# Optimization experiments

Hardware: AMD Instinct MI355X
Metric: run time of the kernel (lower is better)

Reference implementation:

```python
import jax, jax.numpy as jnp
import numpy as np

LN_EPS = 1e-5

def _layer_norm(x, g, b):
    m = jnp.mean(x, axis=-1, keepdims=True)
    v = jnp.mean((x - m) ** 2, axis=-1, keepdims=True)
    return (x - m) / jnp.sqrt(v + LN_EPS) * g + b

def setup_inputs() -> dict:
    key = jax.random.key(0)
    ks = jax.random.split(key, 16)
    B, L, D = 4, 2048, 1024
    DF = 4 * D
    s_in = 1.0 / np.sqrt(D)
    s_ff = 1.0 / np.sqrt(DF)
    # torch init of phazor: exp(2j*pi*arange(D)/D) * |randn|
    ang = 2.0 * np.pi * jnp.arange(D, dtype=jnp.float32) / D
    mag = jnp.abs(jax.random.normal(ks[0], (D,), jnp.float32))
    return {
        "x": jax.random.normal(ks[1], (B, L, D), jnp.float32),
        "hidden_real": jax.random.normal(ks[2], (B, D), jnp.float32),
        "hidden_imag": jax.random.normal(ks[3], (B, D), jnp.float32),
        "phazor_real": mag * jnp.cos(ang),
        "phazor_imag": mag * jnp.sin(ang),
        "phazor_init_real": jax.random.normal(ks[4], (D,), jnp.float32),
        "phazor_init_imag": jax.random.normal(ks[5], (D,), jnp.float32),
        "ln_gamma": jnp.ones((D,), jnp.float32),
        "ln_beta": jnp.zeros((D,), jnp.float32),
        "fc_w": jax.random.uniform(ks[6], (D, D), jnp.float32, -s_in, s_in),
        "fc_b": jax.random.uniform(ks[7], (D,), jnp.float32, -s_in, s_in),
        "w1": jax.random.uniform(ks[8], (DF, D), jnp.float32, -s_in, s_in),
        "b1": jax.random.uniform(ks[9], (DF,), jnp.float32, -s_in, s_in),
        "w2": jax.random.uniform(ks[10], (D, DF), jnp.float32, -s_ff, s_ff),
        "b2": jax.random.uniform(ks[11], (D,), jnp.float32, -s_ff, s_ff),
    }

def _spiral_conv(x, hidden, phazor_p, phazor_init):
    # x: [B,L,D] real, hidden: [B,D] complex
    B, L, D = x.shape
    amag = jnp.abs(phazor_p)
    phazor = phazor_p / amag * jnp.exp(-amag)                      # [D]
    prog = jnp.power(phazor[None, :], jnp.arange(L)[:, None])      # [L,D]
    filt = prog * phazor_init[None, :]                             # [L,D]
    filt_fft = jnp.fft.fft(filt, n=2 * L, axis=0)                  # [2L,D]
    x_fft = jnp.fft.fft(x.astype(jnp.complex64), n=2 * L, axis=1)  # [B,2L,D]
    conv = jnp.fft.ifft(filt_fft[None] * x_fft, axis=1)[:, :L]     # [B,L,D]
    conv_with_past = conv + jax.lax.stop_gradient(hidden)[:, None, :] * prog[None] * phazor[None, None]
    return conv_with_past.real, conv_with_past

def reference(x, hidden_real, hidden_imag, phazor_real, phazor_imag,
              phazor_init_real, phazor_init_imag, ln_gamma, ln_beta,
              fc_w, fc_b, w1, b1, w2, b2):
    hidden = hidden_real + 1j * hidden_imag
    phazor_p = phazor_real + 1j * phazor_imag
    phazor_init = phazor_init_real + 1j * phazor_init_imag

    x_res = x
    xn = _layer_norm(x, ln_gamma, ln_beta)
    s, new_hidden = _spiral_conv(xn, hidden, phazor_p, phazor_init)
    y = jax.nn.silu(jnp.einsum('bld,ed->ble', x, fc_w) + fc_b)
    h = s * y + x_res                      # dropout is identity (p=0 / eval)
    hn = _layer_norm(h, ln_gamma, ln_beta) # same LayerNorm instance reused
    ffn = jnp.einsum('blf,df->bld', jax.nn.silu(jnp.einsum('bld,fd->blf', hn, w1) + b1), w2) + b2
    out = ffn + h
    return out, new_hidden
```

## Files before the change

### kernel.cpp

```cpp
#include <hip/hip_runtime.h>

typedef unsigned short u16;
typedef unsigned int u32;
typedef float f32x4 __attribute__((ext_vector_type(4)));
typedef __bf16 bf16x8 __attribute__((ext_vector_type(8)));

__device__ __forceinline__ float b2f(u16 u) {
    return __uint_as_float(((u32)u) << 16);
}
__device__ __forceinline__ u16 f2b(float f) {
    u32 u = __float_as_uint(f);
    return (u16)((u + 0x7FFFu + ((u >> 16) & 1u)) >> 16);
}
__device__ __forceinline__ bool is_f32(const u32* flag) {
    return flag[0] == 0x3F800000u;
}
__device__ __forceinline__ float lda(const void* p, size_t i, bool f) {
    return f ? ((const float*)p)[i] : b2f(((const u16*)p)[i]);
}
__device__ __forceinline__ void cmul(float& xr, float& xi, float yr, float yi) {
    float tr = xr * yr - xi * yi;
    xi = xr * yi + xi * yr;
    xr = tr;
}
__device__ __forceinline__ void gl2lds16(const void* g, void* l) {
    __builtin_amdgcn_global_load_lds(
        (const __attribute__((address_space(1))) void*)g,
        (__attribute__((address_space(3))) void*)l, 16, 0, 0);
}
__device__ __forceinline__ void wg_barrier() {
    asm volatile("" ::: "memory");
    __builtin_amdgcn_sched_barrier(0);
    __builtin_amdgcn_s_barrier();
    __builtin_amdgcn_sched_barrier(0);
    asm volatile("" ::: "memory");
}
#define VWAIT0 { asm volatile("s_waitcnt vmcnt(0)" ::: "memory"); __builtin_amdgcn_sched_barrier(0); }
#define VWAIT6 { asm volatile("s_waitcnt vmcnt(6)" ::: "memory"); __builtin_amdgcn_sched_barrier(0); }

__global__ __launch_bounds__(256) void cvt_k(const void* __restrict__ src,
                                             u32* __restrict__ dst, int n2,
                                             const u32* __restrict__ flag) {
    bool f = is_f32(flag);
    int i = blockIdx.x * 256 + threadIdx.x;
    if (i >= n2) return;
    if (f) {
        float2 v = ((const float2*)src)[i];
        dst[i] = (u32)f2b(v.x) | ((u32)f2b(v.y) << 16);
    } else {
        dst[i] = ((const u32*)src)[i];
    }
}

__global__ __launch_bounds__(256) void ln_k(const u16* __restrict__ x,
                                            const u16* __restrict__ g,
                                            const u16* __restrict__ be,
                                            u16* __restrict__ o, int D) {
    int row = blockIdx.x;
    const u16* xr = x + (size_t)row * D;
    int tid = threadIdx.x;
    float s = 0.f, s2 = 0.f;
    for (int i = tid; i < D; i += 256) {
        float v = b2f(xr[i]);
        s += v; s2 += v * v;
    }
    for (int off = 32; off > 0; off >>= 1) {
        s  += __shfl_down(s,  off, 64);
        s2 += __shfl_down(s2, off, 64);
    }
    __shared__ float red[8];
    int wave = tid >> 6;
    if ((tid & 63) == 0) { red[wave * 2] = s; red[wave * 2 + 1] = s2; }
    __syncthreads();
    if (tid == 0) {
        float ts = 0.f, ts2 = 0.f;
        for (int w = 0; w < 4; w++) { ts += red[w * 2]; ts2 += red[w * 2 + 1]; }
        float m = ts / D;
        float v = ts2 / D - m * m;
        red[0] = m;
        red[1] = rsqrtf(v + 1e-5f);
    }
    __syncthreads();
    float m = red[0], inv = red[1];
    u16* orow = o + (size_t)row * D;
    for (int i = tid; i < D; i += 256) {
        float v = (b2f(xr[i]) - m) * inv * b2f(g[i]) + b2f(be[i]);
        orow[i] = f2b(v);
    }
}

__global__ __launch_bounds__(256) void scan_partial_k(const u16* __restrict__ xn,
                                                      const void* __restrict__ phr_,
                                                      const void* __restrict__ phi_,
                                                      float2* __restrict__ T,
                                                      int L, int D, int C, int Kc,
                                                      const u32* __restrict__ flag) {
    bool f = is_f32(flag);
    int tid = blockIdx.x * 256 + threadIdx.x;
    int d = tid % D;
    int c = (tid / D) % C;
    int b = tid / (D * C);
    float pr = lda(phr_, d, f), pi = lda(phi_, d, f);
    float amag = fmaxf(sqrtf(pr * pr + pi * pi), 1e-12f);
    float sc = __expf(-amag) / amag;
    float phr = pr * sc, phi = pi * sc;
    float Tr = 0.f, Ti = 0.f;
    const u16* xp = xn + ((size_t)b * L + (size_t)c * Kc) * D + d;
    for (int t = 0; t < Kc; t++) {
        float x = b2f(xp[(size_t)t * D]);
        float nr = phr * Tr - phi * Ti + x;
        Ti = phr * Ti + phi * Tr;
        Tr = nr;
    }
    T[tid] = make_float2(Tr, Ti);
}

__global__ __launch_bounds__(256) void scan_prefix_k(const void* __restrict__ phr_,
                                                     const void* __restrict__ phi_,
                                                     const float2* __restrict__ T,
                                                     float2* __restrict__ E,
                                                     int D, int C,
                                                     const u32* __restrict__ flag) {
    bool f = is_f32(flag);
    int tid = blockIdx.x * 256 + threadIdx.x;
    int d = tid % D;
    int b = tid / D;
    float pr = lda(phr_, d, f), pi = lda(phi_, d, f);
    float amag = fmaxf(sqrtf(pr * pr + pi * pi), 1e-12f);
    float sc = __expf(-amag) / amag;
    float phr = pr * sc, phi = pi * sc;
    float kr = phr, ki = phi;
    for (int s = 0; s < 7; s++) cmul(kr, ki, kr, ki);
    float cr = 0.f, ci = 0.f;
    for (int c = 0; c < C; c++) {
        size_t i = ((size_t)b * C + c) * D + d;
        E[i] = make_float2(cr, ci);
        float2 t = T[i];
        cmul(cr, ci, kr, ki);
        cr += t.x; ci += t.y;
    }
}

__global__ __launch_bounds__(256) void scan_final_k(const u16* __restrict__ xn,
                                                    const void* __restrict__ phr_,
                                                    const void* __restrict__ phi_,
                                                    const void* __restrict__ pir_,
                                                    const void* __restrict__ pii_,
                                                    const void* __restrict__ hr_,
                                                    const void* __restrict__ hi_,
                                                    const float2* __restrict__ E,
                                                    u16* __restrict__ sws,
                                                    void* __restrict__ dout,
                                                    int MD, int out_elems,
                                                    int L, int D, int C, int Kc,
                                                    const u32* __restrict__ flag) {
    bool f = is_f32(flag);
    int tid = blockIdx.x * 256 + threadIdx.x;
    int d = tid % D;
    int c = (tid / D) % C;
    int b = tid / (D * C);
    float pr = lda(phr_, d, f), pi = lda(phi_, d, f);
    float amag = fmaxf(sqrtf(pr * pr + pi * pi), 1e-12f);
    float sc = __expf(-amag) / amag;
    float phr = pr * sc, phi = pi * sc;
    float kr = phr, ki = phi;
    for (int s = 0; s < 7; s++) cmul(kr, ki, kr, ki);
    float Pr = phr, Pi = phi;
    for (int j = 0; j < c; j++) cmul(Pr, Pi, kr, ki);
    float ir = lda(pir_, d, f), ii = lda(pii_, d, f);
    float hr = lda(hr_, (size_t)b * D + d, f), hi = lda(hi_, (size_t)b * D + d, f);
    float2 e = E[tid];
    float Sr = e.x, Si = e.y;
    const bool full = (out_elems >= 3 * MD);
    size_t mbase = (size_t)b * L + (size_t)c * Kc;
    for (int t = 0; t < Kc; t++) {
        size_t off = (mbase + t) * D + d;
        float x = b2f(xn[off]);
        float nr = phr * Sr - phi * Si + x;
        Si = phr * Si + phi * Sr;
        Sr = nr;
        float cr = ir * Sr - ii * Si + hr * Pr - hi * Pi;
        float ci = ir * Si + ii * Sr + hr * Pi + hi * Pr;
        sws[off] = f2b(cr);
        if (f) {
            float* fo = (float*)dout;
            if (full) {
                fo[(size_t)MD + 2 * off]     = cr;
                fo[(size_t)MD + 2 * off + 1] = ci;
            } else {
                fo[(size_t)MD + off] = cr;
            }
        } else {
            u16* uo = (u16*)dout;
            if (full) {
                uo[(size_t)MD + 2 * off]     = f2b(cr);
                uo[(size_t)MD + 2 * off + 1] = f2b(ci);
            } else {
                uo[(size_t)MD + off] = f2b(cr);
            }
        }
        cmul(Pr, Pi, phr, phi);
    }
}

template <int MODE>
__global__ __launch_bounds__(512) void gemm_nt(const u16* __restrict__ A,
                                               const u16* __restrict__ Bm,
                                               int M, int N, int K,
                                               const u16* __restrict__ bias,
                                               const u16* __restrict__ sbuf,
                                               const u16* __restrict__ xbuf,
                                               u16* __restrict__ out,
                                               void* __restrict__ outv,
                                               const u32* __restrict__ flag) {
    __shared__ u16 As[3][128 * 64];
    __shared__ u16 Bs[3][256 * 64];
    const int tid = threadIdx.x;
    const int wave = tid >> 6, lane = tid & 63;
    const int quad = lane >> 4, l16 = lane & 15;

    const int NT = N >> 8;
    const int j = blockIdx.x;
    const int gsize = 8 * NT;
    const int mg  = j / gsize;
    const int rem = j - mg * gsize;
    const int nt  = rem >> 3;
    const int mi  = rem & 7;
    const int bm = (mg * 8 + mi) * 128, bn = nt * 256;

    const int wrow = (wave >> 2) * 64, wcol = (wave & 3) * 64;

    f32x4 acc[4][4] = {};

    const int lr = lane >> 3;
    const int sl = (lane & 7) ^ lr;
    const size_t goff = (size_t)lr * K + sl * 8;
    const u16* aG = A  + (size_t)(bm + wave * 16) * K + goff;
    const u16* bG = Bm + (size_t)(bn + wave * 32) * K + goff;
    const size_t K8 = (size_t)K * 8;

    u16* aB0 = &As[0][0]; u16* aB1 = &As[1][0]; u16* aB2 = &As[2][0];
    u16* bB0 = &Bs[0][0]; u16* bB1 = &Bs[1][0]; u16* bB2 = &Bs[2][0];

#define STG_P1(aB, bB, t) { \
        const u16* ga = aG + (size_t)(t) * 64; \
        gl2lds16(ga,      (aB) + wave * (16 * 64)); \
        gl2lds16(ga + K8, (aB) + wave * (16 * 64) + 8 * 64); \
        gl2lds16(bG + (size_t)(t) * 64, (bB) + wave * (32 * 64)); }
#define STG_P2(bB, t) { \
        const u16* gb = bG + (size_t)(t) * 64; \
        gl2lds16(gb + K8,     (bB) + wave * (32 * 64) + 8 * 64); \
        gl2lds16(gb + 2 * K8, (bB) + wave * (32 * 64) + 16 * 64); \
        gl2lds16(gb + 3 * K8, (bB) + wave * (32 * 64) + 24 * 64); }

#define RDA(aB, m, ks) (*(const bf16x8*)&(aB)[(wrow + (m) * 16 + l16) * 64 + \
        ((((ks) * 4 + quad) ^ (l16 & 7)) << 3)])
#define RDB(bB, n, ks) (*(const bf16x8*)&(bB)[(wcol + (n) * 16 + l16) * 64 + \
        ((((ks) * 4 + quad) ^ (l16 & 7)) << 3)])

#define FM(mm, nn, ks) acc[mm][nn] = __builtin_amdgcn_mfma_f32_16x16x32_bf16( \
        av[mm][ks], bv[nn][ks], acc[mm][nn], 0, 0, 0)
#define MFMA16(ks) { \
        __builtin_amdgcn_s_setprio(1); \
        FM(0, 0, ks); FM(0, 1, ks); FM(1, 0, ks); FM(1, 1, ks); \
        FM(0, 2, ks); FM(0, 3, ks); FM(1, 2, ks); FM(1, 3, ks); \
        FM(2, 0, ks); FM(2, 1, ks); FM(3, 0, ks); FM(3, 1, ks); \
        FM(2, 2, ks); FM(2, 3, ks); FM(3, 2, ks); FM(3, 3, ks); \
        __builtin_amdgcn_s_setprio(0); }

    bf16x8 av[4][2], bv[4][2];
    const int KT = K >> 6;

    STG_P1(aB0, bB0, 0); STG_P2(bB0, 0);
    STG_P1(aB1, bB1, 1); STG_P2(bB1, 1);
    VWAIT6;
    wg_barrier();

    for (int t = 0; t < KT; ++t) {
        const bool stg = (t + 2 < KT);
        av[0][0] = RDA(aB0, 0, 0); av[1][0] = RDA(aB0, 1, 0);
        av[2][0] = RDA(aB0, 2, 0); av[3][0] = RDA(aB0, 3, 0);
        bv[0][0] = RDB(bB0, 0, 0); bv[1][0] = RDB(bB0, 1, 0);
        bv[2][0] = RDB(bB0, 2, 0); bv[3][0] = RDB(bB0, 3, 0);
        if (stg) STG_P1(aB2, bB2, t + 2);
        wg_barrier();
        MFMA16(0);
        wg_barrier();
        av[0][1] = RDA(aB0, 0, 1); av[1][1] = RDA(aB0, 1, 1);
        av[2][1] = RDA(aB0, 2, 1); av[3][1] = RDA(aB0, 3, 1);
        bv[0][1] = RDB(bB0, 0, 1); bv[1][1] = RDB(bB0, 1, 1);
        bv[2][1] = RDB(bB0, 2, 1); bv[3][1] = RDB(bB0, 3, 1);
        if (stg) STG_P2(bB2, t + 2);
        wg_barrier();
        MFMA16(1);
        if (stg) { VWAIT6 }
        else if (t + 1 < KT) { VWAIT0 }
        wg_barrier();
        u16* ta = aB0; aB0 = aB1; aB1 = aB2; aB2 = ta;
        u16* tb = bB0; bB0 = bB1; bB1 = bB2; bB2 = tb;
    }

    bool f = (MODE == 2) ? is_f32(flag) : false;
#pragma unroll
    for (int mi2 = 0; mi2 < 4; mi2++) {
#pragma unroll
        for (int ni = 0; ni < 4; ni++) {
            int colg = bn + wcol + ni * 16 + l16;
            float bsv = b2f(bias[colg]);
#pragma unroll
            for (int r = 0; r < 4; r++) {
                int rowg = bm + wrow + mi2 * 16 + quad * 4 + r;
                size_t idx = (size_t)rowg * N + colg;
                float v = acc[mi2][ni][r] + bsv;
                if (MODE == 0) {
                    float y = v / (1.f + __expf(-v));
                    float hv = b2f(sbuf[idx]) * y + b2f(xbuf[idx]);
                    out[idx] = f2b(hv);
                } else if (MODE == 1) {
                    float y = v / (1.f + __expf(-v));
                    out[idx] = f2b(y);
                } else {
                    float o = v + b2f(xbuf[idx]);
                    if (f) ((float*)outv)[idx] = o;
                    else   ((u16*)outv)[idx] = f2b(o);
                }
            }
        }
    }
#undef STG_P1
#undef STG_P2
#undef RDA
#undef RDB
#undef FM
#undef MFMA16
}

extern "C" void kernel_launch(void* const* d_in, const int* in_sizes, int n_in,
                              void* d_out, int out_size, void* d_ws, size_t ws_size,
                              hipStream_t stream) {
    const void* x   = d_in[0];
    const void* hr  = d_in[1];
    const void* hi  = d_in[2];
    const void* phr = d_in[3];
    const void* phi = d_in[4];
    const void* pir = d_in[5];
    const void* pii = d_in[6];
    const void* g   = d_in[7];
    const void* be  = d_in[8];
    const void* fcw = d_in[9];
    const void* fcb = d_in[10];
    const void* w1  = d_in[11];
    const void* b1  = d_in[12];
    const void* w2  = d_in[13];
    const void* b2  = d_in[14];
    const u32* flag = (const u32*)g;

    const int D  = in_sizes[3];
    const int Bb = in_sizes[1] / D;
    const int L  = in_sizes[0] / (Bb * D);
    const int DF = in_sizes[12];
    const int M  = Bb * L;
    const int Kc = 128, C = L / Kc;
    const int MD = M * D;

    char* ws = (char*)d_ws;
    size_t MD2 = (size_t)MD * 2;
    u16*    xb  = (u16*)(ws);
    u16*    xn  = (u16*)(ws + MD2);
    u16*    sws = (u16*)(ws + 2 * MD2);
    float2* T   = (float2*)(ws + 3 * MD2);
    float2* E   = (float2*)(ws + 3 * MD2 + (size_t)Bb * C * D * 8);
    u16*    a1  = (u16*)(ws);
    u16*    h   = (u16*)(ws + 4 * MD2);
    u16*    hn  = (u16*)(ws + 5 * MD2);
    char*   wp  = ws + 6 * MD2;
    u16* fcwb = (u16*)wp; wp += (size_t)D * D * 2;
    u16* w1b  = (u16*)wp; wp += (size_t)DF * D * 2;
    u16* w2b  = (u16*)wp; wp += (size_t)D * DF * 2;
    u16* fcbb = (u16*)wp; wp += (size_t)D * 2;
    u16* b1b  = (u16*)wp; wp += (size_t)DF * 2;
    u16* b2b  = (u16*)wp; wp += (size_t)D * 2;
    u16* gb   = (u16*)wp; wp += (size_t)D * 2;
    u16* bb   = (u16*)wp; wp += (size_t)D * 2;

    auto cvt = [&](const void* src, u16* dst, size_t n) {
        int n2 = (int)(n / 2);
        cvt_k<<<(n2 + 255) / 256, 256, 0, stream>>>(src, (u32*)dst, n2, flag);
    };
    cvt(x,   xb,   (size_t)MD);
    cvt(fcw, fcwb, (size_t)D * D);
    cvt(w1,  w1b,  (size_t)DF * D);
    cvt(w2,  w2b,  (size_t)D * DF);
    cvt(fcb, fcbb, (size_t)D);
    cvt(b1,  b1b,  (size_t)DF);
    cvt(b2,  b2b,  (size_t)D);
    cvt(g,   gb,   (size_t)D);
    cvt(be,  bb,   (size_t)D);

    ln_k<<<M, 256, 0, stream>>>(xb, gb, bb, xn, D);
    scan_partial_k<<<(Bb * C * D) / 256, 256, 0, stream>>>(xn, phr, phi, T, L, D, C, Kc, flag);
    scan_prefix_k<<<(Bb * D) / 256, 256, 0, stream>>>(phr, phi, T, E, D, C, flag);
    scan_final_k<<<(Bb * C * D) / 256, 256, 0, stream>>>(xn, phr, phi, pir, pii, hr, hi,
                                                         E, sws, d_out, MD, out_size,
                                                         L, D, C, Kc, flag);
    gemm_nt<0><<<(M / 128) * (D / 256), 512, 0, stream>>>(xb, fcwb, M, D, D, fcbb, sws, xb, h, nullptr, flag);
    ln_k<<<M, 256, 0, stream>>>(h, gb, bb, hn, D);
    gemm_nt<1><<<(M / 128) * (DF / 256), 512, 0, stream>>>(hn, w1b, M, DF, D, b1b, nullptr, nullptr, a1, nullptr, flag);
    gemm_nt<2><<<(M / 128) * (D / 256), 512, 0, stream>>>(a1, w2b, M, D, DF, b2b, nullptr, h, nullptr, d_out, flag);
}
```

Before: 472.8 us.

## Unroll GEMM K-loop by three with static LDS buffers and one barrier per step

Replaces the rotating LDS buffer pointers with compile-time buffer indices by unrolling the K loop three ways. Each K step now issues the whole next-stage global-to-LDS copy at once, reads both k-slices of fragments up front, then runs 32 MFMAs behind a single barrier instead of three. This cuts barrier count and pointer arithmetic and may let the compiler schedule LDS reads better. In exchange it uses more registers and code size and waits longer before the first MFMA of each step.

```diff
diff --git a/kernel.cpp b/kernel.cpp
--- a/kernel.cpp
+++ b/kernel.cpp
@@ -239,23 +239,19 @@
     const u16* bG = Bm + (size_t)(bn + wave * 32) * K + goff;
     const size_t K8 = (size_t)K * 8;
 
-    u16* aB0 = &As[0][0]; u16* aB1 = &As[1][0]; u16* aB2 = &As[2][0];
-    u16* bB0 = &Bs[0][0]; u16* bB1 = &Bs[1][0]; u16* bB2 = &Bs[2][0];
-
-#define STG_P1(aB, bB, t) { \
+#define STG(B, t) { \
         const u16* ga = aG + (size_t)(t) * 64; \
-        gl2lds16(ga,      (aB) + wave * (16 * 64)); \
-        gl2lds16(ga + K8, (aB) + wave * (16 * 64) + 8 * 64); \
-        gl2lds16(bG + (size_t)(t) * 64, (bB) + wave * (32 * 64)); }
-#define STG_P2(bB, t) { \
         const u16* gb = bG + (size_t)(t) * 64; \
-        gl2lds16(gb + K8,     (bB) + wave * (32 * 64) + 8 * 64); \
-        gl2lds16(gb + 2 * K8, (bB) + wave * (32 * 64) + 16 * 64); \
-        gl2lds16(gb + 3 * K8, (bB) + wave * (32 * 64) + 24 * 64); }
-
-#define RDA(aB, m, ks) (*(const bf16x8*)&(aB)[(wrow + (m) * 16 + l16) * 64 + \
+        gl2lds16(ga,          &As[B][wave * (16 * 64)]); \
+        gl2lds16(ga + K8,     &As[B][wave * (16 * 64) + 8 * 64]); \
+        gl2lds16(gb,          &Bs[B][wave * (32 * 64)]); \
+        gl2lds16(gb + K8,     &Bs[B][wave * (32 * 64) + 8 * 64]); \
+        gl2lds16(gb + 2 * K8, &Bs[B][wave * (32 * 64) + 16 * 64]); \
+        gl2lds16(gb + 3 * K8, &Bs[B][wave * (32 * 64) + 24 * 64]); }
+
+#define RDA(B, m, ks) (*(const bf16x8*)&As[B][(wrow + (m) * 16 + l16) * 64 + \
         ((((ks) * 4 + quad) ^ (l16 & 7)) << 3)])
-#define RDB(bB, n, ks) (*(const bf16x8*)&(bB)[(wcol + (n) * 16 + l16) * 64 + \
+#define RDB(B, n, ks) (*(const bf16x8*)&Bs[B][(wcol + (n) * 16 + l16) * 64 + \
         ((((ks) * 4 + quad) ^ (l16 & 7)) << 3)])
 
 #define FM(mm, nn, ks) acc[mm][nn] = __builtin_amdgcn_mfma_f32_16x16x32_bf16( \
@@ -268,36 +264,34 @@
         FM(2, 2, ks); FM(2, 3, ks); FM(3, 2, ks); FM(3, 3, ks); \
         __builtin_amdgcn_s_setprio(0); }
 
+#define ITER(RB, SB, t) { \
+        if ((t) + 2 < KT) STG(SB, (t) + 2); \
+        av[0][0] = RDA(RB, 0, 0); av[1][0] = RDA(RB, 1, 0); \
+        av[2][0] = RDA(RB, 2, 0); av[3][0] = RDA(RB, 3, 0); \
+        bv[0][0] = RDB(RB, 0, 0); bv[1][0] = RDB(RB, 1, 0); \
+        bv[2][0] = RDB(RB, 2, 0); bv[3][0] = RDB(RB, 3, 0); \
+        av[0][1] = RDA(RB, 0, 1); av[1][1] = RDA(RB, 1, 1); \
+        av[2][1] = RDA(RB, 2, 1); av[3][1] = RDA(RB, 3, 1); \
+        bv[0][1] = RDB(RB, 0, 1); bv[1][1] = RDB(RB, 1, 1); \
+        bv[2][1] = RDB(RB, 2, 1); bv[3][1] = RDB(RB, 3, 1); \
+        MFMA16(0); \
+        MFMA16(1); \
+        if ((t) + 2 < KT) { VWAIT6 } \
+        else if ((t) + 1 < KT) { VWAIT0 } \
+        wg_barrier(); }
+
     bf16x8 av[4][2], bv[4][2];
     const int KT = K >> 6;
 
-    STG_P1(aB0, bB0, 0); STG_P2(bB0, 0);
-    STG_P1(aB1, bB1, 1); STG_P2(bB1, 1);
+    STG(0, 0);
+    STG(1, 1);
     VWAIT6;
     wg_barrier();
 
-    for (int t = 0; t < KT; ++t) {
-        const bool stg = (t + 2 < KT);
-        av[0][0] = RDA(aB0, 0, 0); av[1][0] = RDA(aB0, 1, 0);
-        av[2][0] = RDA(aB0, 2, 0); av[3][0] = RDA(aB0, 3, 0);
-        bv[0][0] = RDB(bB0, 0, 0); bv[1][0] = RDB(bB0, 1, 0);
-        bv[2][0] = RDB(bB0, 2, 0); bv[3][0] = RDB(bB0, 3, 0);
-        if (stg) STG_P1(aB2, bB2, t + 2);
-        wg_barrier();
-        MFMA16(0);
-        wg_barrier();
-        av[0][1] = RDA(aB0, 0, 1); av[1][1] = RDA(aB0, 1, 1);
-        av[2][1] = RDA(aB0, 2, 1); av[3][1] = RDA(aB0, 3, 1);
-        bv[0][1] = RDB(bB0, 0, 1); bv[1][1] = RDB(bB0, 1, 1);
-        bv[2][1] = RDB(bB0, 2, 1); bv[3][1] = RDB(bB0, 3, 1);
-        if (stg) STG_P2(bB2, t + 2);
-        wg_barrier();
-        MFMA16(1);
-        if (stg) { VWAIT6 }
-        else if (t + 1 < KT) { VWAIT0 }
-        wg_barrier();
-        u16* ta = aB0; aB0 = aB1; aB1 = aB2; aB2 = ta;
-        u16* tb = bB0; bB0 = bB1; bB1 = bB2; bB2 = tb;
+    for (int tb = 0; tb < KT; tb += 3) {
+        ITER(0, 2, tb);
+        if (tb + 1 < KT) ITER(1, 0, tb + 1);
+        if (tb + 2 < KT) ITER(2, 1, tb + 2);
     }
 
     bool f = (MODE == 2) ? is_f32(flag) : false;
@@ -327,12 +321,12 @@
             }
         }
     }
-#undef STG_P1
-#undef STG_P2
+#undef STG
 #undef RDA
 #undef RDB
 #undef FM
 #undef MFMA16
+#undef ITER
 }
 
 extern "C" void kernel_launch(void* const* d_in, const int* in_sizes, int n_in,
```

Measured after the change: 500.3 us. 5.8% more time.
